# Performance work log

Hardware: AMD Instinct MI355X
Metric: run time of the kernel (lower is better)

Reference implementation:

```python
import jax, jax.numpy as jnp
import numpy as np
import math

EPS = 1e-5  # torch LayerNorm default
B, T, H, W, C = 2, 16, 32, 32, 768
NH = 12
HD = C // NH


def layernorm(x, w, b):
    mu = jnp.mean(x, axis=-1, keepdims=True)
    var = jnp.var(x, axis=-1, keepdims=True)
    return (x - mu) * jax.lax.rsqrt(var + EPS) * w + b


def setup_inputs() -> dict:
    key = jax.random.key(0)
    ks = jax.random.split(key, 4)
    s = 1.0 / math.sqrt(C)
    return {
        "x": jax.random.normal(ks[0], (B, T, H, W, C), dtype=jnp.float32),
        "ln1_w": jnp.ones((C,), jnp.float32),
        "ln1_b": jnp.zeros((C,), jnp.float32),
        "Wqkv": jax.random.normal(ks[1], (3 * C, C), jnp.float32) * s,
        "bqkv": jnp.zeros((3 * C,), jnp.float32),
        "ln2_w": jnp.ones((C,), jnp.float32),
        "ln2_b": jnp.zeros((C,), jnp.float32),
        "Wout": jax.random.normal(ks[2], (C, C), jnp.float32) * s,
        "bout": jnp.zeros((C,), jnp.float32),
    }


def reference(x, ln1_w, ln1_b, Wqkv, bqkv, ln2_w, ln2_b, Wout, bout):
    b, t, h, w, c = x.shape
    inp = x
    y = layernorm(x, ln1_w, ln1_b)
    qkv = jnp.einsum('bthwc,fc->bthwf', y, Wqkv) + bqkv          # (B,T,H,W,3C)
    qkv = qkv.reshape(b, t, h, w, NH, 3 * HD)
    q, k, v = jnp.split(qkv, 3, axis=-1)                          # each (B,T,H,W,NH,HD)
    scale = 1.0 / math.sqrt(HD)
    # attention over the time axis, batched over (b,h,w,heads)
    scores = jnp.einsum('bthwnd,bshwnd->bhwnts', q, k) * scale    # (B,H,W,NH,T,T)
    attn = jax.nn.softmax(scores, axis=-1)
    o = jnp.einsum('bhwnts,bshwnd->bthwnd', attn, v)              # (B,T,H,W,NH,HD)
    o = o.reshape(b, t, h, w, c)
    o = layernorm(o, ln2_w, ln2_b)
    o = jnp.einsum('bthwc,fc->bthwf', o, Wout) + bout
    return o + inp
```

## Files before the change

### kernel.cpp

```cpp
#include <hip/hip_runtime.h>

typedef unsigned short u16;
typedef __attribute__((ext_vector_type(8))) short frag8;
typedef __attribute__((ext_vector_type(4))) float f32x4;

static constexpr int C = 768;
static constexpr int F3 = 2304;
static constexpr int MROWS = 32768;
static constexpr float LNEPS = 1e-5f;

__device__ __forceinline__ float bfu2f(u16 u){
  union { unsigned u; float f; } x; x.u = (unsigned)u << 16; return x.f;
}
__device__ __forceinline__ u16 f2bfu(float f){
  union { float f; unsigned u; } x; x.f = f;
  unsigned r = x.u + 0x7fffu + ((x.u >> 16) & 1u);
  return (u16)(r >> 16);
}

__device__ __forceinline__ void gload16(const void* g, void* l){
  __builtin_amdgcn_global_load_lds(
      (const __attribute__((address_space(1))) void*)g,
      (__attribute__((address_space(3))) void*)l, 16, 0, 0);
}

__global__ __launch_bounds__(256) void cvt_bf16(const float* __restrict__ src,
                                                u16* __restrict__ dst, int n){
  int i = blockIdx.x * 256 + threadIdx.x;
  if (i < n) dst[i] = f2bfu(src[i]);
}

__global__ __launch_bounds__(256) void ln1_kernel(const float* __restrict__ x,
    const float* __restrict__ w, const float* __restrict__ b, u16* __restrict__ y){
  const int lane = threadIdx.x & 63, wid = threadIdx.x >> 6;
  const size_t row = (size_t)blockIdx.x * 4 + wid;
  const float4* xr = reinterpret_cast<const float4*>(x + row * C);
  float v[12];
  #pragma unroll
  for (int j = 0; j < 3; j++){
    float4 t = xr[lane + j*64];
    v[j*4+0]=t.x; v[j*4+1]=t.y; v[j*4+2]=t.z; v[j*4+3]=t.w;
  }
  float s = 0.f, ss = 0.f;
  #pragma unroll
  for (int j = 0; j < 12; j++){ s += v[j]; ss += v[j]*v[j]; }
  #pragma unroll
  for (int o = 32; o; o >>= 1){ s += __shfl_xor(s, o, 64); ss += __shfl_xor(ss, o, 64); }
  const float mu = s * (1.f/768.f);
  const float rs = rsqrtf(ss*(1.f/768.f) - mu*mu + LNEPS);
  ushort4* yr = reinterpret_cast<ushort4*>(y + row * C);
  const float4* wv = reinterpret_cast<const float4*>(w);
  const float4* bv = reinterpret_cast<const float4*>(b);
  #pragma unroll
  for (int j = 0; j < 3; j++){
    float4 wj = wv[lane + j*64], bj = bv[lane + j*64];
    ushort4 o4;
    o4.x = f2bfu((v[j*4+0]-mu)*rs*wj.x + bj.x);
    o4.y = f2bfu((v[j*4+1]-mu)*rs*wj.y + bj.y);
    o4.z = f2bfu((v[j*4+2]-mu)*rs*wj.z + bj.z);
    o4.w = f2bfu((v[j*4+3]-mu)*rs*wj.w + bj.w);
    yr[lane + j*64] = o4;
  }
}

template<int MODE>
__device__ __forceinline__ void gemm_body(
    const u16* __restrict__ A, const u16* __restrict__ Bw,
    const float* __restrict__ bias, const float* __restrict__ resid,
    void* __restrict__ Cout, int Ndim, int K)
{
  __shared__ __align__(16) char lds[49152];
  const int tid = threadIdx.x;
  const int lane = tid & 63, wn = tid >> 6;
  const int ntn = Ndim >> 8;
  const int cpx = (int)gridDim.x >> 3;
  const int wg = ((int)blockIdx.x & 7) * cpx + ((int)blockIdx.x >> 3);
  const int bm = wg / ntn, bn = wg % ntn;
  const int m0 = bm << 7, n0 = bn << 8;

  const int rp = lane >> 2;
  const int rr = rp ^ ((rp >> 2) & 1);
  const int qq = (lane & 3) ^ (rr & 3);
  const u16* aS = A  + (size_t)(m0 + rr) * K + qq*8;
  const u16* bS = Bw + (size_t)(n0 + rr) * K + qq*8;
  const size_t rgK = 16 * (size_t)K;

  const int fr = lane & 15, kq = lane >> 4;
  const int sig16 = (((fr ^ ((fr >> 2) & 1)) << 2) | (kq ^ (fr & 3))) * 16;

  f32x4 acc[8][4] = {};

  auto stage = [&](int ts){
    char* lb = lds + (ts & 1)*24576;
    const u16* a = aS + ts*32;
    const u16* b = bS + ts*32;
    gload16(a + (size_t)(2*wn    )*rgK, lb + (2*wn    )*1024);
    gload16(a + (size_t)(2*wn + 1)*rgK, lb + (2*wn + 1)*1024);
    #pragma unroll
    for (int i = 0; i < 4; i++)
      gload16(b + (size_t)(4*wn + i)*rgK, lb + 8192 + (4*wn + i)*1024);
  };

  stage(0);

  for (int t = 0; t < 24; ++t){
    int tn = t + 1; if (tn >= 24) tn = 0;
    stage(tn);
    asm volatile("s_waitcnt vmcnt(6)" ::: "memory");
    __builtin_amdgcn_s_barrier();

    const char* base = lds + (t & 1)*24576;
    const char* pb = base + 8192 + (wn*4)*1024 + sig16;
    frag8 af[8], bf[4];
    #pragma unroll
    for (int nf = 0; nf < 4; nf++) bf[nf] = *reinterpret_cast<const frag8*>(pb + nf*1024);
    #pragma unroll
    for (int mf = 0; mf < 8; mf++) af[mf] = *reinterpret_cast<const frag8*>(base + mf*1024 + sig16);
    asm volatile("s_waitcnt lgkmcnt(0)" ::: "memory");
    __builtin_amdgcn_sched_barrier(0);
    __builtin_amdgcn_s_setprio(1);
    #pragma unroll
    for (int mf = 0; mf < 8; mf++)
      #pragma unroll
      for (int nf = 0; nf < 4; nf++)
        acc[mf][nf] = __builtin_amdgcn_mfma_f32_16x16x32_bf16(bf[nf], af[mf], acc[mf][nf], 0, 0, 0);
    __builtin_amdgcn_s_setprio(0);
    __builtin_amdgcn_s_barrier();
  }
  asm volatile("s_waitcnt vmcnt(0)" ::: "memory");

  const int em = fr, en = kq * 4;
  float4 bb[4];
  #pragma unroll
  for (int nf = 0; nf < 4; nf++)
    bb[nf] = *reinterpret_cast<const float4*>(bias + n0 + wn*64 + nf*16 + en);

  #pragma unroll
  for (int mf = 0; mf < 8; mf++){
    const size_t m = (size_t)(m0 + mf*16 + em);
    #pragma unroll
    for (int nf = 0; nf < 4; nf++){
      const int n = n0 + wn*64 + nf*16 + en;
      if (MODE == 0){
        ushort4 o4;
        o4.x = f2bfu(acc[mf][nf][0] + bb[nf].x);
        o4.y = f2bfu(acc[mf][nf][1] + bb[nf].y);
        o4.z = f2bfu(acc[mf][nf][2] + bb[nf].z);
        o4.w = f2bfu(acc[mf][nf][3] + bb[nf].w);
        *reinterpret_cast<ushort4*>((u16*)Cout + m * Ndim + n) = o4;
      } else {
        const float4 rr4 = *reinterpret_cast<const float4*>(resid + m * Ndim + n);
        float4 o4;
        o4.x = acc[mf][nf][0] + bb[nf].x + rr4.x;
        o4.y = acc[mf][nf][1] + bb[nf].y + rr4.y;
        o4.z = acc[mf][nf][2] + bb[nf].z + rr4.z;
        o4.w = acc[mf][nf][3] + bb[nf].w + rr4.w;
        *reinterpret_cast<float4*>((float*)Cout + m * Ndim + n) = o4;
      }
    }
  }
}

__global__ __launch_bounds__(256, 2) void gemm_qkv(
    const u16* __restrict__ A, const u16* __restrict__ Bw,
    const float* __restrict__ bias, void* __restrict__ Cout, int Ndim, int K){
  gemm_body<0>(A, Bw, bias, nullptr, Cout, Ndim, K);
}
__global__ __launch_bounds__(256, 2) void gemm_out(
    const u16* __restrict__ A, const u16* __restrict__ Bw,
    const float* __restrict__ bias, const float* __restrict__ resid,
    void* __restrict__ Cout, int Ndim, int K){
  gemm_body<1>(A, Bw, bias, resid, Cout, Ndim, K);
}

__global__ __launch_bounds__(256, 3) void attn_ln2(const u16* __restrict__ qkv,
    const float* __restrict__ w2, const float* __restrict__ b2, u16* __restrict__ y2){
  __shared__ __align__(16) u16 Obuf[16][772];
  __shared__ __align__(16) u16 Vt[13864];
  const int tid = threadIdx.x;
  const int lane = tid & 63, wid = tid >> 6;
  const int bid = blockIdx.x;
  const int w = bid & 31, h = (bid >> 5) & 31, b = bid >> 10;
  const size_t rbase = (size_t)b*16384 + h*32 + w;

  #pragma unroll
  for (int i = 0; i < 4; i++){
    const int idx = tid + i*256;
    if (idx < 786){
      int off;
      if (idx < 780){
        const int n = idx / 65, r = idx - n*65;
        off = (r < 64) ? (n*1154 + r*18 + 16) : (n*1154 + 1152);
      } else {
        off = 13848 + (idx - 780)*2;
      }
      *reinterpret_cast<unsigned*>(&Vt[off]) = 0u;
    }
  }

  #pragma unroll
  for (int it = 0; it < 6; it++){
    const int e = tid + it*256;
    const int t = e / 96, c = e % 96;
    const int n = c >> 3, j = c & 7;
    union { uint4 u; u16 s[8]; } vv;
    vv.u = *reinterpret_cast<const uint4*>(qkv + (rbase + (size_t)t*1024)*F3 + (n*24 + 16 + j)*8);
    #pragma unroll
    for (int x = 0; x < 8; x++)
      Vt[n*1154 + (j*8 + x)*18 + t] = vv.s[x];
  }
  __syncthreads();

  const int q = lane >> 4, tcol = lane & 15;
  const u16* gq = qkv + (rbase + (size_t)tcol*1024)*F3;

  #pragma unroll
  for (int hh = 0; hh < 3; hh++){
    const int n = wid*3 + hh;
    const frag8 qf0 = *reinterpret_cast<const frag8*>(gq + (n*24 +  0 + q)*8);
    const frag8 qf1 = *reinterpret_cast<const frag8*>(gq + (n*24 +  4 + q)*8);
    const frag8 kf0 = *reinterpret_cast<const frag8*>(gq + (n*24 +  8 + q)*8);
    const frag8 kf1 = *reinterpret_cast<const frag8*>(gq + (n*24 + 12 + q)*8);
    f32x4 sa = {};
    sa = __builtin_amdgcn_mfma_f32_16x16x32_bf16(kf0, qf0, sa, 0, 0, 0);
    sa = __builtin_amdgcn_mfma_f32_16x16x32_bf16(kf1, qf1, sa, 0, 0, 0);
    const float sc0 = sa[0]*0.125f, sc1 = sa[1]*0.125f;
    const float sc2 = sa[2]*0.125f, sc3 = sa[3]*0.125f;
    float mx = fmaxf(fmaxf(sc0, sc1), fmaxf(sc2, sc3));
    mx = fmaxf(mx, __shfl_xor(mx, 16, 64));
    mx = fmaxf(mx, __shfl_xor(mx, 32, 64));
    float p0 = __expf(sc0-mx), p1 = __expf(sc1-mx), p2 = __expf(sc2-mx), p3 = __expf(sc3-mx);
    float sm = p0+p1+p2+p3;
    sm += __shfl_xor(sm, 16, 64);
    sm += __shfl_xor(sm, 32, 64);
    const float inv = 1.f / sm;
    const unsigned b0 = (unsigned)f2bfu(p0*inv) | ((unsigned)f2bfu(p1*inv) << 16);
    const unsigned b1 = (unsigned)f2bfu(p2*inv) | ((unsigned)f2bfu(p3*inv) << 16);
    const unsigned t0 = __shfl((unsigned)b0, (lane+16)&63, 64);
    const unsigned t1 = __shfl((unsigned)b1, (lane+16)&63, 64);
    const unsigned t2 = __shfl((unsigned)b0, (lane+32)&63, 64);
    const unsigned t3 = __shfl((unsigned)b1, (lane+32)&63, 64);
    union { frag8 f; unsigned u[4]; } pu;
    pu.u[0] = (q==0) ? b0 : ((q==1) ? t0 : 0u);
    pu.u[1] = (q==0) ? b1 : ((q==1) ? t1 : 0u);
    pu.u[2] = (q==0) ? t0 : ((q==1) ? t2 : 0u);
    pu.u[3] = (q==0) ? t1 : ((q==1) ? t3 : 0u);

    #pragma unroll
    for (int dcv = 0; dcv < 4; dcv++){
      union { frag8 f; unsigned u[4]; } vf;
      const int vi = n*1154 + (dcv*16 + tcol)*18 + q*8;
      #pragma unroll
      for (int i2 = 0; i2 < 4; i2++)
        vf.u[i2] = *reinterpret_cast<const unsigned*>(&Vt[vi + 2*i2]);
      f32x4 oa = {};
      oa = __builtin_amdgcn_mfma_f32_16x16x32_bf16(vf.f, pu.f, oa, 0, 0, 0);
      uint2 ow;
      ow.x = (unsigned)f2bfu(oa[0]) | ((unsigned)f2bfu(oa[1]) << 16);
      ow.y = (unsigned)f2bfu(oa[2]) | ((unsigned)f2bfu(oa[3]) << 16);
      *reinterpret_cast<uint2*>(&Obuf[tcol][n*64 + dcv*16 + q*4]) = ow;
    }
  }
  __syncthreads();

  #pragma unroll
  for (int rq = 0; rq < 4; rq++){
    const int t = wid*4 + rq;
    float v[12];
    #pragma unroll
    for (int j = 0; j < 12; j++) v[j] = bfu2f(Obuf[t][j*64 + lane]);
    float s = 0.f, ss = 0.f;
    #pragma unroll
    for (int j = 0; j < 12; j++){ s += v[j]; ss += v[j]*v[j]; }
    #pragma unroll
    for (int o = 32; o; o >>= 1){ s += __shfl_xor(s, o, 64); ss += __shfl_xor(ss, o, 64); }
    const float mu = s * (1.f/768.f);
    const float rs = rsqrtf(ss*(1.f/768.f) - mu*mu + LNEPS);
    u16* yr = y2 + (rbase + (size_t)t*1024) * C;
    #pragma unroll
    for (int j = 0; j < 12; j++){
      const int c = j*64 + lane;
      yr[c] = f2bfu((v[j]-mu)*rs*w2[c] + b2[c]);
    }
  }
}

extern "C" void kernel_launch(void* const* d_in, const int* in_sizes, int n_in,
                              void* d_out, int out_size, void* d_ws, size_t ws_size,
                              hipStream_t stream){
  const float* x    = (const float*)d_in[0];
  const float* ln1w = (const float*)d_in[1];
  const float* ln1b = (const float*)d_in[2];
  const float* Wqkv = (const float*)d_in[3];
  const float* bqkv = (const float*)d_in[4];
  const float* ln2w = (const float*)d_in[5];
  const float* ln2b = (const float*)d_in[6];
  const float* Wout = (const float*)d_in[7];
  const float* bout = (const float*)d_in[8];
  float* out = (float*)d_out;

  char* ws = (char*)d_ws;
  u16* qkv = (u16*)ws;
  u16* y   = (u16*)(ws + 150994944);
  u16* wq  = (u16*)(ws + 201326592);
  u16* wo  = (u16*)(ws + 204865536);

  cvt_bf16<<<(F3*C + 255)/256, 256, 0, stream>>>(Wqkv, wq, F3*C);
  cvt_bf16<<<(C*C + 255)/256, 256, 0, stream>>>(Wout, wo, C*C);
  ln1_kernel<<<MROWS/4, 256, 0, stream>>>(x, ln1w, ln1b, y);
  gemm_qkv<<<(MROWS/128)*(F3/256), 256, 0, stream>>>(y, wq, bqkv, qkv, F3, C);
  attn_ln2<<<2*32*32, 256, 0, stream>>>(qkv, ln2w, ln2b, y);
  gemm_out<<<(MROWS/128)*(C/256), 256, 0, stream>>>(y, wo, bout, x, out, C, C);
}
```

Measured before the change: 305.6 us.

## Triple-buffer LDS and prefetch next fragments during MFMA in GEMM

Moves the GEMM main loop from double- to triple-buffered LDS staging with global loads issued two tiles ahead. LDS fragment reads for the next k-step are issued before the current step's MFMAs, using ping-pong register sets. The goal is to hide global-load and LDS-read latency behind matrix math. The cost is 72KB of LDS per block, which can reduce occupancy, plus roughly double the fragment registers, which adds register pressure. It also removes the trailing barrier, so buffer-reuse safety now depends on the three-deep rotation.

```diff
diff --git a/kernel.cpp b/kernel.cpp
--- a/kernel.cpp
+++ b/kernel.cpp
@@ -69,7 +69,7 @@
     const float* __restrict__ bias, const float* __restrict__ resid,
     void* __restrict__ Cout, int Ndim, int K)
 {
-  __shared__ __align__(16) char lds[49152];
+  __shared__ __align__(16) char lds[73728];
   const int tid = threadIdx.x;
   const int lane = tid & 63, wn = tid >> 6;
   const int ntn = Ndim >> 8;
@@ -91,7 +91,7 @@
   f32x4 acc[8][4] = {};
 
   auto stage = [&](int ts){
-    char* lb = lds + (ts & 1)*24576;
+    char* lb = lds + (ts % 3)*24576;
     const u16* a = aS + ts*32;
     const u16* b = bS + ts*32;
     gload16(a + (size_t)(2*wn    )*rgK, lb + (2*wn    )*1024);
@@ -100,24 +100,15 @@
     for (int i = 0; i < 4; i++)
       gload16(b + (size_t)(4*wn + i)*rgK, lb + 8192 + (4*wn + i)*1024);
   };
-
-  stage(0);
-
-  for (int t = 0; t < 24; ++t){
-    int tn = t + 1; if (tn >= 24) tn = 0;
-    stage(tn);
-    asm volatile("s_waitcnt vmcnt(6)" ::: "memory");
-    __builtin_amdgcn_s_barrier();
-
-    const char* base = lds + (t & 1)*24576;
+  auto readFrags = [&](int ts, frag8 (&af)[8], frag8 (&bf)[4]){
+    const char* base = lds + (ts % 3)*24576;
     const char* pb = base + 8192 + (wn*4)*1024 + sig16;
-    frag8 af[8], bf[4];
     #pragma unroll
     for (int nf = 0; nf < 4; nf++) bf[nf] = *reinterpret_cast<const frag8*>(pb + nf*1024);
     #pragma unroll
     for (int mf = 0; mf < 8; mf++) af[mf] = *reinterpret_cast<const frag8*>(base + mf*1024 + sig16);
-    asm volatile("s_waitcnt lgkmcnt(0)" ::: "memory");
-    __builtin_amdgcn_sched_barrier(0);
+  };
+  auto domfma = [&](frag8 (&af)[8], frag8 (&bf)[4]){
     __builtin_amdgcn_s_setprio(1);
     #pragma unroll
     for (int mf = 0; mf < 8; mf++)
@@ -125,7 +116,33 @@
       for (int nf = 0; nf < 4; nf++)
         acc[mf][nf] = __builtin_amdgcn_mfma_f32_16x16x32_bf16(bf[nf], af[mf], acc[mf][nf], 0, 0, 0);
     __builtin_amdgcn_s_setprio(0);
+  };
+
+  frag8 afA[8], bfA[4], afB[8], bfB[4];
+
+  stage(0); stage(1);
+  asm volatile("s_waitcnt vmcnt(6)" ::: "memory");
+  __builtin_amdgcn_s_barrier();
+  readFrags(0, afA, bfA);
+  asm volatile("s_waitcnt lgkmcnt(0)" ::: "memory");
+  __builtin_amdgcn_sched_barrier(0);
+
+  auto step = [&](int t, frag8 (&afC)[8], frag8 (&bfC)[4],
+                  frag8 (&afN)[8], frag8 (&bfN)[4]){
+    int ts = t + 2; if (ts >= 24) ts -= 24;
+    stage(ts);
+    asm volatile("s_waitcnt vmcnt(6)" ::: "memory");
     __builtin_amdgcn_s_barrier();
+    int tn = t + 1;
+    readFrags(tn == 24 ? 0 : tn, afN, bfN);
+    domfma(afC, bfC);
+    asm volatile("s_waitcnt lgkmcnt(0)" ::: "memory");
+    __builtin_amdgcn_sched_barrier(0);
+  };
+
+  for (int t = 0; t < 24; t += 2){
+    step(t,     afA, bfA, afB, bfB);
+    step(t + 1, afB, bfB, afA, bfA);
   }
   asm volatile("s_waitcnt vmcnt(0)" ::: "memory");
 
```

Result: no change. 308.5 us (+0.9%).

## Use 128x128 tiles with 2x2 wave layout for output GEMM; prefetch QK loads

Applied to the files above, without the earlier changes.

Splits the shared GEMM template into two kernels. The output projection now uses 128x128 tiles with a 2x2 wave grid, 32KB of LDS and occupancy 3, and its grid doubles to 1536 blocks, which should fill the GPU better for the N=768 case. The attention kernel software-pipelines the per-head Q/K fragment loads, so the next head's global loads are issued before the current head's compute. In exchange, the smaller tiles reuse each loaded operand less, and the prefetch raises register pressure.

```diff
diff --git a/kernel.cpp b/kernel.cpp
--- a/kernel.cpp
+++ b/kernel.cpp
@@ -63,11 +63,9 @@
   }
 }
 
-template<int MODE>
-__device__ __forceinline__ void gemm_body(
+__global__ __launch_bounds__(256, 2) void gemm_qkv(
     const u16* __restrict__ A, const u16* __restrict__ Bw,
-    const float* __restrict__ bias, const float* __restrict__ resid,
-    void* __restrict__ Cout, int Ndim, int K)
+    const float* __restrict__ bias, u16* __restrict__ Cout, int Ndim, int K)
 {
   __shared__ __align__(16) char lds[49152];
   const int tid = threadIdx.x;
@@ -141,36 +139,106 @@
     #pragma unroll
     for (int nf = 0; nf < 4; nf++){
       const int n = n0 + wn*64 + nf*16 + en;
-      if (MODE == 0){
-        ushort4 o4;
-        o4.x = f2bfu(acc[mf][nf][0] + bb[nf].x);
-        o4.y = f2bfu(acc[mf][nf][1] + bb[nf].y);
-        o4.z = f2bfu(acc[mf][nf][2] + bb[nf].z);
-        o4.w = f2bfu(acc[mf][nf][3] + bb[nf].w);
-        *reinterpret_cast<ushort4*>((u16*)Cout + m * Ndim + n) = o4;
-      } else {
-        const float4 rr4 = *reinterpret_cast<const float4*>(resid + m * Ndim + n);
-        float4 o4;
-        o4.x = acc[mf][nf][0] + bb[nf].x + rr4.x;
-        o4.y = acc[mf][nf][1] + bb[nf].y + rr4.y;
-        o4.z = acc[mf][nf][2] + bb[nf].z + rr4.z;
-        o4.w = acc[mf][nf][3] + bb[nf].w + rr4.w;
-        *reinterpret_cast<float4*>((float*)Cout + m * Ndim + n) = o4;
-      }
-    }
-  }
-}
-
-__global__ __launch_bounds__(256, 2) void gemm_qkv(
-    const u16* __restrict__ A, const u16* __restrict__ Bw,
-    const float* __restrict__ bias, void* __restrict__ Cout, int Ndim, int K){
-  gemm_body<0>(A, Bw, bias, nullptr, Cout, Ndim, K);
-}
-__global__ __launch_bounds__(256, 2) void gemm_out(
+      ushort4 o4;
+      o4.x = f2bfu(acc[mf][nf][0] + bb[nf].x);
+      o4.y = f2bfu(acc[mf][nf][1] + bb[nf].y);
+      o4.z = f2bfu(acc[mf][nf][2] + bb[nf].z);
+      o4.w = f2bfu(acc[mf][nf][3] + bb[nf].w);
+      *reinterpret_cast<ushort4*>(Cout + m * Ndim + n) = o4;
+    }
+  }
+}
+
+__global__ __launch_bounds__(256, 3) void gemm_out(
     const u16* __restrict__ A, const u16* __restrict__ Bw,
     const float* __restrict__ bias, const float* __restrict__ resid,
-    void* __restrict__ Cout, int Ndim, int K){
-  gemm_body<1>(A, Bw, bias, resid, Cout, Ndim, K);
+    float* __restrict__ Cout, int Ndim, int K)
+{
+  __shared__ __align__(16) char lds[32768];
+  const int tid = threadIdx.x;
+  const int lane = tid & 63, wid = tid >> 6;
+  const int wm = wid >> 1, wn = wid & 1;
+  const int ntn = Ndim >> 7;
+  const int cpx = (int)gridDim.x >> 3;
+  const int wg = ((int)blockIdx.x & 7) * cpx + ((int)blockIdx.x >> 3);
+  const int bm = wg / ntn, bn = wg % ntn;
+  const int m0 = bm << 7, n0 = bn << 7;
+
+  const int rp = lane >> 2;
+  const int rr = rp ^ ((rp >> 2) & 1);
+  const int qq = (lane & 3) ^ (rr & 3);
+  const u16* aS = A  + (size_t)(m0 + rr) * K + qq*8;
+  const u16* bS = Bw + (size_t)(n0 + rr) * K + qq*8;
+  const size_t rgK = 16 * (size_t)K;
+
+  const int fr = lane & 15, kq = lane >> 4;
+  const int sig16 = (((fr ^ ((fr >> 2) & 1)) << 2) | (kq ^ (fr & 3))) * 16;
+
+  f32x4 acc[4][4] = {};
+
+  auto stage = [&](int ts){
+    char* lb = lds + (ts & 1)*16384;
+    const u16* a = aS + ts*32;
+    const u16* b = bS + ts*32;
+    gload16(a + (size_t)wid       * rgK, lb + wid*1024);
+    gload16(a + (size_t)(wid + 4) * rgK, lb + (wid+4)*1024);
+    gload16(b + (size_t)wid       * rgK, lb + 8192 + wid*1024);
+    gload16(b + (size_t)(wid + 4) * rgK, lb + 8192 + (wid+4)*1024);
+  };
+
+  stage(0);
+
+  for (int t = 0; t < 24; ++t){
+    int tn = t + 1; if (tn >= 24) tn = 0;
+    stage(tn);
+    asm volatile("s_waitcnt vmcnt(4)" ::: "memory");
+    __builtin_amdgcn_s_barrier();
+
+    const char* base = lds + (t & 1)*16384;
+    const char* pa = base + (wm*4)*1024 + sig16;
+    const char* pb = base + 8192 + (wn*4)*1024 + sig16;
+    frag8 af[4], bf[4];
+    #pragma unroll
+    for (int nf = 0; nf < 4; nf++) bf[nf] = *reinterpret_cast<const frag8*>(pb + nf*1024);
+    #pragma unroll
+    for (int mf = 0; mf < 4; mf++) af[mf] = *reinterpret_cast<const frag8*>(pa + mf*1024);
+    asm volatile("s_waitcnt lgkmcnt(0)" ::: "memory");
+    __builtin_amdgcn_sched_barrier(0);
+    __builtin_amdgcn_s_setprio(1);
+    #pragma unroll
+    for (int mf = 0; mf < 4; mf++)
+      #pragma unroll
+      for (int nf = 0; nf < 4; nf++)
+        acc[mf][nf] = __builtin_amdgcn_mfma_f32_16x16x32_bf16(bf[nf], af[mf], acc[mf][nf], 0, 0, 0);
+    __builtin_amdgcn_s_setprio(0);
+    __builtin_amdgcn_s_barrier();
+  }
+  asm volatile("s_waitcnt vmcnt(0)" ::: "memory");
+
+  const int em = fr, en = kq * 4;
+  float4 bb[2];
+  #pragma unroll
+  for (int nf = 0; nf < 2; nf++){}
+  float4 bb4[4];
+  #pragma unroll
+  for (int nf = 0; nf < 4; nf++)
+    bb4[nf] = *reinterpret_cast<const float4*>(bias + n0 + wn*64 + nf*16 + en);
+
+  #pragma unroll
+  for (int mf = 0; mf < 4; mf++){
+    const size_t m = (size_t)(m0 + wm*64 + mf*16 + em);
+    #pragma unroll
+    for (int nf = 0; nf < 4; nf++){
+      const int n = n0 + wn*64 + nf*16 + en;
+      const float4 rr4 = *reinterpret_cast<const float4*>(resid + m * Ndim + n);
+      float4 o4;
+      o4.x = acc[mf][nf][0] + bb4[nf].x + rr4.x;
+      o4.y = acc[mf][nf][1] + bb4[nf].y + rr4.y;
+      o4.z = acc[mf][nf][2] + bb4[nf].z + rr4.z;
+      o4.w = acc[mf][nf][3] + bb4[nf].w + rr4.w;
+      *reinterpret_cast<float4*>(Cout + m * Ndim + n) = o4;
+    }
+  }
 }
 
 __global__ __launch_bounds__(256, 3) void attn_ln2(const u16* __restrict__ qkv,
@@ -214,13 +282,14 @@
   const int q = lane >> 4, tcol = lane & 15;
   const u16* gq = qkv + (rbase + (size_t)tcol*1024)*F3;
 
-  #pragma unroll
-  for (int hh = 0; hh < 3; hh++){
-    const int n = wid*3 + hh;
-    const frag8 qf0 = *reinterpret_cast<const frag8*>(gq + (n*24 +  0 + q)*8);
-    const frag8 qf1 = *reinterpret_cast<const frag8*>(gq + (n*24 +  4 + q)*8);
-    const frag8 kf0 = *reinterpret_cast<const frag8*>(gq + (n*24 +  8 + q)*8);
-    const frag8 kf1 = *reinterpret_cast<const frag8*>(gq + (n*24 + 12 + q)*8);
+  auto ldqk = [&](int n, frag8& q0, frag8& q1, frag8& k0, frag8& k1){
+    q0 = *reinterpret_cast<const frag8*>(gq + (n*24 +  0 + q)*8);
+    q1 = *reinterpret_cast<const frag8*>(gq + (n*24 +  4 + q)*8);
+    k0 = *reinterpret_cast<const frag8*>(gq + (n*24 +  8 + q)*8);
+    k1 = *reinterpret_cast<const frag8*>(gq + (n*24 + 12 + q)*8);
+  };
+
+  auto headCompute = [&](int n, frag8 qf0, frag8 qf1, frag8 kf0, frag8 kf1){
     f32x4 sa = {};
     sa = __builtin_amdgcn_mfma_f32_16x16x32_bf16(kf0, qf0, sa, 0, 0, 0);
     sa = __builtin_amdgcn_mfma_f32_16x16x32_bf16(kf1, qf1, sa, 0, 0, 0);
@@ -234,15 +303,15 @@
     sm += __shfl_xor(sm, 16, 64);
     sm += __shfl_xor(sm, 32, 64);
     const float inv = 1.f / sm;
-    const unsigned b0 = (unsigned)f2bfu(p0*inv) | ((unsigned)f2bfu(p1*inv) << 16);
-    const unsigned b1 = (unsigned)f2bfu(p2*inv) | ((unsigned)f2bfu(p3*inv) << 16);
-    const unsigned t0 = __shfl((unsigned)b0, (lane+16)&63, 64);
-    const unsigned t1 = __shfl((unsigned)b1, (lane+16)&63, 64);
-    const unsigned t2 = __shfl((unsigned)b0, (lane+32)&63, 64);
-    const unsigned t3 = __shfl((unsigned)b1, (lane+32)&63, 64);
+    const unsigned c0 = (unsigned)f2bfu(p0*inv) | ((unsigned)f2bfu(p1*inv) << 16);
+    const unsigned c1 = (unsigned)f2bfu(p2*inv) | ((unsigned)f2bfu(p3*inv) << 16);
+    const unsigned t0 = __shfl((unsigned)c0, (lane+16)&63, 64);
+    const unsigned t1 = __shfl((unsigned)c1, (lane+16)&63, 64);
+    const unsigned t2 = __shfl((unsigned)c0, (lane+32)&63, 64);
+    const unsigned t3 = __shfl((unsigned)c1, (lane+32)&63, 64);
     union { frag8 f; unsigned u[4]; } pu;
-    pu.u[0] = (q==0) ? b0 : ((q==1) ? t0 : 0u);
-    pu.u[1] = (q==0) ? b1 : ((q==1) ? t1 : 0u);
+    pu.u[0] = (q==0) ? c0 : ((q==1) ? t0 : 0u);
+    pu.u[1] = (q==0) ? c1 : ((q==1) ? t1 : 0u);
     pu.u[2] = (q==0) ? t0 : ((q==1) ? t2 : 0u);
     pu.u[3] = (q==0) ? t1 : ((q==1) ? t3 : 0u);
 
@@ -260,7 +329,15 @@
       ow.y = (unsigned)f2bfu(oa[2]) | ((unsigned)f2bfu(oa[3]) << 16);
       *reinterpret_cast<uint2*>(&Obuf[tcol][n*64 + dcv*16 + q*4]) = ow;
     }
-  }
+  };
+
+  frag8 a0, a1, a2, a3, p0, p1, p2, p3;
+  ldqk(wid*3 + 0, a0, a1, a2, a3);
+  ldqk(wid*3 + 1, p0, p1, p2, p3);
+  headCompute(wid*3 + 0, a0, a1, a2, a3);
+  ldqk(wid*3 + 2, a0, a1, a2, a3);
+  headCompute(wid*3 + 1, p0, p1, p2, p3);
+  headCompute(wid*3 + 2, a0, a1, a2, a3);
   __syncthreads();
 
   #pragma unroll
@@ -310,5 +387,5 @@
   ln1_kernel<<<MROWS/4, 256, 0, stream>>>(x, ln1w, ln1b, y);
   gemm_qkv<<<(MROWS/128)*(F3/256), 256, 0, stream>>>(y, wq, bqkv, qkv, F3, C);
   attn_ln2<<<2*32*32, 256, 0, stream>>>(qkv, ln2w, ln2b, y);
-  gemm_out<<<(MROWS/128)*(C/256), 256, 0, stream>>>(y, wo, bout, x, out, C, C);
-}
+  gemm_out<<<(MROWS/128)*(C/128), 256, 0, stream>>>(y, wo, bout, x, out, C, C);
+}
```

New measurement: 308.5 us. About the same (+0.9%).
